# Kernel tuning notes

Measured on AMD Instinct MI355X. Metric: run time of the kernel, lower is better.

## Reference

```python
import jax, jax.numpy as jnp
import numpy as np

SCALE = 56  # output spatial resolution, HW = 3136
K = 3       # n_neighbors for top-k softmin scoring


def avg_pool3(x):
    # F.avg_pool2d(x, 3, 1, 1) with count_include_pad=True -> zero-padded sum / 9
    s = jax.lax.reduce_window(x, 0.0, jax.lax.add, (1, 1, 3, 3), (1, 1, 1, 1),
                              ((0, 0), (0, 0), (1, 1), (1, 1)))
    return s / 9.0


def resize_to(x, hw):
    # F.interpolate(mode='bilinear', align_corners=False) == jax.image half-pixel bilinear
    B, C, _, _ = x.shape
    return jax.image.resize(x, (B, C, hw, hw), method='bilinear')


def add_coords(x):
    # CoordConv AddCoords: append normalized x/y coordinate channels in [-1, 1]
    B, C, H, W = x.shape
    xx = jnp.broadcast_to(jnp.linspace(-1.0, 1.0, W, dtype=x.dtype)[None, :], (H, W))
    yy = jnp.broadcast_to(jnp.linspace(-1.0, 1.0, H, dtype=x.dtype)[:, None], (H, W))
    xxb = jnp.broadcast_to(xx[None, None], (B, 1, H, W))
    yyb = jnp.broadcast_to(yy[None, None], (B, 1, H, W))
    return jnp.concatenate([x, xxb, yyb], axis=1)


def setup_inputs() -> dict:
    key = jax.random.key(0)
    k1, k2, k3, k4, k5 = jax.random.split(key, 5)
    p1 = jax.random.normal(k1, (8, 256, 56, 56), dtype=jnp.float32)
    p2 = jax.random.normal(k2, (8, 512, 28, 28), dtype=jnp.float32)
    p3 = jax.random.normal(k3, (8, 1024, 14, 14), dtype=jnp.float32)
    W = jax.random.normal(k4, (1792, 1794), dtype=jnp.float32) * 0.02  # 1x1 CoordConv weight
    b = jnp.zeros((1792,), dtype=jnp.float32)
    C = jax.random.normal(k5, (1792, 3136), dtype=jnp.float32) * 0.05  # centroid bank
    return {"p1": p1, "p2": p2, "p3": p3, "W": W, "b": b, "C": C}


def reference(p1, p2, p3, W, b, C):
    # Descriptor: smooth each pyramid level, upsample to 56x56, concat -> (B,1792,56,56)
    o1 = avg_pool3(p1)
    o2 = resize_to(avg_pool3(p2), SCALE)
    o3 = resize_to(avg_pool3(p3), SCALE)
    sample = jnp.concatenate([o1, o2, o3], axis=1)
    # CoordConv 1x1
    xc = add_coords(sample)  # (B, 1794, 56, 56)
    phi = jnp.einsum('bchw,oc->bohw', xc, W) + b[None, :, None, None]
    B = phi.shape[0]
    phi_p = phi.reshape(B, 1792, SCALE * SCALE).transpose(0, 2, 1)  # (B, HW, C)
    # pairwise squared distances via expansion + matmul: (B, HW, 3136)
    features = jnp.sum(phi_p * phi_p, axis=2, keepdims=True)
    centers = jnp.sum(C * C, axis=0, keepdims=True)
    dist = features + centers - 2.0 * jnp.matmul(phi_p, C)
    dist = jnp.sqrt(jnp.maximum(dist, 0.0))
    # top-K smallest distances (ascending, like torch.topk(largest=False))
    vals = -jax.lax.top_k(-dist, K)[0]  # (B, HW, K)
    w = jax.nn.softmax(-vals, axis=-1)  # softmin
    score = w[..., 0] * vals[..., 0]    # (B, HW)
    score = score.reshape(B, 1, SCALE, SCALE)
    return score
```

## Files before the change

kernel.cpp:

```cpp
#include <hip/hip_runtime.h>
#include <math.h>
#include <stdint.h>

typedef float f32x4 __attribute__((ext_vector_type(4)));
typedef short short8 __attribute__((ext_vector_type(8)));

static constexpr int HWo   = 3136;
static constexpr int NB    = 8;
static constexpr int NP    = 3200;
static constexpr int KDIM  = 1794;
static constexpr int KP1   = 1856;
static constexpr int ODIM  = 1792;
static constexpr int NCENT = 3136;
static constexpr int NHB   = 50;
static constexpr int NHBV  = 49;

__device__ __forceinline__ uint16_t f2bf(float f) {
  union { float f; uint32_t u; } v; v.f = f;
  uint32_t u = v.u;
  return (uint16_t)((u + 0x7FFFu + ((u >> 16) & 1u)) >> 16);
}
__device__ __forceinline__ float bf2f(uint16_t h) {
  union { uint32_t u; float f; } v; v.u = ((uint32_t)h) << 16;
  return v.f;
}

__device__ __forceinline__ void gld16(const uint16_t* __restrict__ g, uint16_t* l) {
  __builtin_amdgcn_global_load_lds(
      (const __attribute__((address_space(1))) uint16_t*)g,
      (__attribute__((address_space(3))) uint16_t*)l,
      16, 0, 0);
}

__device__ __forceinline__ int xcd_swizzle(int bid, int nwg) {
  int q = nwg >> 3, r = nwg & 7;
  int xcd = bid & 7, idx = bid >> 3;
  int base = (xcd < r) ? xcd * (q + 1) : r * (q + 1) + (xcd - r) * q;
  return base + idx;
}

__global__ __launch_bounds__(256) void convW_kernel(const float* __restrict__ W, uint16_t* __restrict__ Wh) {
  int idx = blockIdx.x * 256 + threadIdx.x;
  int o = idx / KP1, k = idx % KP1;
  float v = (k < KDIM) ? W[(size_t)o * KDIM + k] : 0.f;
  Wh[idx] = f2bf(v);
}

__global__ __launch_bounds__(256) void convC_kernel(const float* __restrict__ C, uint16_t* __restrict__ Ct) {
  __shared__ float tile[64][65];
  int bj = blockIdx.x * 64;
  int bo = blockIdx.y * 64;
  int tx = threadIdx.x & 63, ty = threadIdx.x >> 6;
  #pragma unroll
  for (int s = 0; s < 16; ++s) {
    int o = ty + s * 4;
    tile[o][tx] = C[(size_t)(bo + o) * NCENT + bj + tx];
  }
  __syncthreads();
  #pragma unroll
  for (int s = 0; s < 16; ++s) {
    int j = ty + s * 4;
    Ct[(size_t)(bj + j) * ODIM + bo + tx] = f2bf(tile[tx][j]);
  }
}

__global__ __launch_bounds__(256) void rownorm_kernel(const uint16_t* __restrict__ src, float* __restrict__ dst) {
  int t = threadIdx.x, lane = t & 63, wave = t >> 6;
  int row = blockIdx.x * 4 + wave;
  const uint32_t* p = (const uint32_t*)(src + (size_t)row * ODIM);
  float s = 0.f;
  #pragma unroll
  for (int it = 0; it < 14; ++it) {
    uint32_t u = p[it * 64 + lane];
    float a = bf2f((uint16_t)(u & 0xFFFF)), b = bf2f((uint16_t)(u >> 16));
    s += a * a + b * b;
  }
  #pragma unroll
  for (int m = 1; m < 64; m <<= 1) s += __shfl_xor(s, m, 64);
  if (lane == 0) dst[row] = s;
}

__global__ __launch_bounds__(256) void zerof_kernel(float* __restrict__ p, int n) {
  int i = blockIdx.x * 256 + threadIdx.x;
  if (i < n) p[i] = 0.f;
}

static constexpr int P1SZ = 256 * 3136;
static constexpr int P2SZ = 512 * 784;
static constexpr int P3SZ = 1024 * 196;
static constexpr int PTOT = P1SZ + P2SZ + P3SZ;

__device__ __forceinline__ float pool9f(const float* __restrict__ p, int S, int y, int x) {
  float s = 0.f;
  for (int dy = -1; dy <= 1; ++dy) {
    int yy = y + dy; if (yy < 0 || yy >= S) continue;
    for (int dx = -1; dx <= 1; ++dx) {
      int xx = x + dx; if (xx < 0 || xx >= S) continue;
      s += p[yy * S + xx];
    }
  }
  return s * (1.f / 9.f);
}

__global__ __launch_bounds__(256) void pool_kernel(const float* __restrict__ p1, const float* __restrict__ p2,
                                                   const float* __restrict__ p3, float* __restrict__ pooled, int g0) {
  int b = g0 + blockIdx.y;
  float* pb = pooled + (size_t)blockIdx.y * PTOT;
  int idx = blockIdx.x * 256 + threadIdx.x;
  const float* src; int S, loc;
  if (idx < P1SZ)              { src = p1 + (size_t)b * P1SZ; S = 56; loc = idx; }
  else if (idx < P1SZ + P2SZ)  { src = p2 + (size_t)b * P2SZ; S = 28; loc = idx - P1SZ; }
  else                         { src = p3 + (size_t)b * P3SZ; S = 14; loc = idx - P1SZ - P2SZ; }
  int c = loc / (S * S), hw = loc % (S * S);
  pb[idx] = pool9f(src + (size_t)c * S * S, S, hw / S, hw % S);
}

__global__ __launch_bounds__(256) void asmA_kernel(const float* __restrict__ pooled, uint16_t* __restrict__ xcb) {
  __shared__ float tile[64][65];
  int bg = blockIdx.z;
  const float* pb = pooled + (size_t)bg * PTOT;
  uint16_t* xb = xcb + (size_t)bg * NP * KP1;
  int p0 = blockIdx.x * 64;
  int c0 = blockIdx.y * 64;
  int tx = threadIdx.x & 63, ty = threadIdx.x >> 6;
  #pragma unroll
  for (int s = 0; s < 16; ++s) {
    int c = ty + s * 4;
    tile[c][tx] = pb[(size_t)(c0 + c) * HWo + p0 + tx];
  }
  __syncthreads();
  #pragma unroll
  for (int s = 0; s < 16; ++s) {
    int p = ty + s * 4;
    xb[(size_t)(p0 + p) * KP1 + c0 + tx] = f2bf(tile[tx][p]);
  }
}

__global__ __launch_bounds__(256) void asmB_kernel(const float* __restrict__ pooled, uint16_t* __restrict__ xcb) {
  __shared__ float rows[2][128][29];
  int bg = blockIdx.z;
  const float* pb = pooled + (size_t)bg * PTOT;
  uint16_t* xb = xcb + (size_t)bg * NP * KP1;
  int y = blockIdx.x;
  int ct = blockIdx.y;
  bool lvl2 = ct < 4;
  int S = lvl2 ? 28 : 14;
  float scale = lvl2 ? 0.5f : 0.25f;
  float shift = lvl2 ? -0.25f : -0.375f;
  int chbase = lvl2 ? 256 + ct * 128 : 768 + (ct - 4) * 128;
  const float* base = lvl2 ? pb + P1SZ + (size_t)(ct * 128) * 784
                           : pb + P1SZ + P2SZ + (size_t)((ct - 4) * 128) * 196;
  int planesz = S * S;
  float sy = y * scale + shift;
  float fy0 = floorf(sy);
  float fy = sy - fy0;
  int y0 = (int)fy0, y1 = y0 + 1;
  y0 = y0 < 0 ? 0 : y0; y1 = y1 > S - 1 ? S - 1 : y1;
  int t = threadIdx.x;
  int tot = 128 * 2 * S;
  for (int idx = t; idx < tot; idx += 256) {
    int r = idx / S, e = idx - r * S;
    int c = r >> 1, yr = r & 1;
    rows[yr][c][e] = base[(size_t)c * planesz + (yr ? y1 : y0) * S + e];
  }
  __syncthreads();
  int c = t & 127, xs = t >> 7;
  #pragma unroll
  for (int xi = 0; xi < 28; ++xi) {
    int x = xi * 2 + xs;
    float sx = x * scale + shift;
    float fx0 = floorf(sx);
    float fx = sx - fx0;
    int x0 = (int)fx0, x1 = x0 + 1;
    x0 = x0 < 0 ? 0 : x0; x1 = x1 > S - 1 ? S - 1 : x1;
    float v00 = rows[0][c][x0], v01 = rows[0][c][x1];
    float v10 = rows[1][c][x0], v11 = rows[1][c][x1];
    float v = (1.f - fy) * ((1.f - fx) * v00 + fx * v01) + fy * ((1.f - fx) * v10 + fx * v11);
    xb[(size_t)(y * 56 + x) * KP1 + chbase + c] = f2bf(v);
  }
}

__global__ __launch_bounds__(256) void asmC_kernel(uint16_t* __restrict__ xcb) {
  int bg = blockIdx.y;
  uint16_t* xb = xcb + (size_t)bg * NP * KP1;
  int idx = blockIdx.x * 256 + threadIdx.x;
  int i = idx >> 6, ch = 1792 + (idx & 63);
  int x = i % 56, y = i / 56;
  float v = (ch == 1792) ? (-1.f + 2.f * x / 55.f)
          : (ch == 1793) ? (-1.f + 2.f * y / 55.f) : 0.f;
  xb[(size_t)i * KP1 + ch] = f2bf(v);
}

__global__ __launch_bounds__(256) void gemm1_mfma(const uint16_t* __restrict__ Wh, const float* __restrict__ bias,
                                                  const uint16_t* __restrict__ xcb, uint16_t* __restrict__ phi_t,
                                                  float* __restrict__ feat) {
  __shared__ union { uint16_t ab[2][128][64]; uint16_t tr[128][136]; } sm;
  int wid = xcd_swizzle(blockIdx.x, gridDim.x);
  int row0 = (wid % 14) * 128;
  int col0 = (wid / 14) * 128;
  int t = threadIdx.x;
  int lane = t & 63, wave = t >> 6;
  int wm = wave & 1, wn = wave >> 1;
  int l15 = lane & 15, quad = lane >> 4;
  int rr = wave * 8 + (lane >> 3);
  int sg = ((lane & 7) ^ (lane >> 3)) * 8;
  f32x4 acc[4][4] = {};
  for (int k0 = 0; k0 < KP1; k0 += 64) {
    #pragma unroll
    for (int i = 0; i < 4; ++i) {
      gld16(&Wh [(size_t)(row0 + i * 32 + rr) * KP1 + k0 + sg], &sm.ab[0][i * 32 + wave * 8][0]);
      gld16(&xcb[(size_t)(col0 + i * 32 + rr) * KP1 + k0 + sg], &sm.ab[1][i * 32 + wave * 8][0]);
    }
    __syncthreads();
    #pragma unroll
    for (int kk = 0; kk < 2; ++kk) {
      short8 a[4], b[4];
      #pragma unroll
      for (int i = 0; i < 4; ++i) {
        int r = wm * 64 + i * 16 + l15;
        a[i] = *(const short8*)&sm.ab[0][r][((quad + 4 * kk) ^ (r & 7)) * 8];
      }
      #pragma unroll
      for (int j = 0; j < 4; ++j) {
        int r = wn * 64 + j * 16 + l15;
        b[j] = *(const short8*)&sm.ab[1][r][((quad + 4 * kk) ^ (r & 7)) * 8];
      }
      #pragma unroll
      for (int i = 0; i < 4; ++i)
        #pragma unroll
        for (int j = 0; j < 4; ++j)
          acc[i][j] = __builtin_amdgcn_mfma_f32_16x16x32_bf16(a[i], b[j], acc[i][j], 0, 0, 0);
    }
    __syncthreads();
  }
  #pragma unroll
  for (int i = 0; i < 4; ++i) {
    int o4 = wm * 64 + i * 16 + quad * 4;
    float4 bv = *(const float4*)&bias[row0 + o4];
    #pragma unroll
    for (int j = 0; j < 4; ++j) {
      int p = wn * 64 + j * 16 + l15;
      ushort4 u;
      u.x = f2bf(acc[i][j][0] + bv.x);
      u.y = f2bf(acc[i][j][1] + bv.y);
      u.z = f2bf(acc[i][j][2] + bv.z);
      u.w = f2bf(acc[i][j][3] + bv.w);
      *(ushort4*)&sm.tr[p][o4] = u;
    }
  }
  __syncthreads();
  int c = t & 15, prb = t >> 4;
  #pragma unroll
  for (int s = 0; s < 8; ++s) {
    int pr = s * 16 + prb;
    uint4 v = *(const uint4*)&sm.tr[pr][c * 8];
    *(uint4*)&phi_t[(size_t)(col0 + pr) * ODIM + row0 + c * 8] = v;
    const uint16_t* pv = (const uint16_t*)&v;
    float ssq = 0.f;
    #pragma unroll
    for (int e = 0; e < 8; ++e) { float f = bf2f(pv[e]); ssq += f * f; }
    #pragma unroll
    for (int m = 1; m < 16; m <<= 1) ssq += __shfl_xor(ssq, m, 16);
    if (c == 0) atomicAdd(&feat[col0 + pr], ssq);
  }
}

__device__ __forceinline__ void ins3(float v, float& a, float& b, float& c) {
  if (v < c) {
    if (v < b) { c = b; if (v < a) { b = a; a = v; } else { b = v; } }
    else { c = v; }
  }
}

__global__ __launch_bounds__(256) void gemm2_mfma(const uint16_t* __restrict__ phi_t, const uint16_t* __restrict__ Ct,
                                                  const float* __restrict__ cent, float* __restrict__ partial) {
  __shared__ uint16_t As[128][64];
  __shared__ uint16_t Bs[128][64];
  int wid = xcd_swizzle(blockIdx.x, gridDim.x);
  int col0 = (wid % 25) * 128;
  int row0 = (wid / 25) * 128;
  int t = threadIdx.x;
  int lane = t & 63, wave = t >> 6;
  int wc = wave & 1;
  int wp = wave >> 1;
  int l15 = lane & 15, quad = lane >> 4;
  int rr = wave * 8 + (lane >> 3);
  int sg = ((lane & 7) ^ (lane >> 3)) * 8;
  f32x4 acc[4][4] = {};
  for (int k0 = 0; k0 < ODIM; k0 += 64) {
    #pragma unroll
    for (int i = 0; i < 4; ++i) {
      gld16(&phi_t[(size_t)(row0 + i * 32 + rr) * ODIM + k0 + sg], &As[i * 32 + wave * 8][0]);
      gld16(&Ct   [(size_t)(col0 + i * 32 + rr) * ODIM + k0 + sg], &Bs[i * 32 + wave * 8][0]);
    }
    __syncthreads();
    #pragma unroll
    for (int kk = 0; kk < 2; ++kk) {
      short8 ac[4], bp[4];
      #pragma unroll
      for (int i = 0; i < 4; ++i) {
        int r = wc * 64 + i * 16 + l15;
        ac[i] = *(const short8*)&Bs[r][((quad + 4 * kk) ^ (r & 7)) * 8];
      }
      #pragma unroll
      for (int j = 0; j < 4; ++j) {
        int r = wp * 64 + j * 16 + l15;
        bp[j] = *(const short8*)&As[r][((quad + 4 * kk) ^ (r & 7)) * 8];
      }
      #pragma unroll
      for (int i = 0; i < 4; ++i)
        #pragma unroll
        for (int j = 0; j < 4; ++j)
          acc[i][j] = __builtin_amdgcn_mfma_f32_16x16x32_bf16(ac[i], bp[j], acc[i][j], 0, 0, 0);
    }
    __syncthreads();
  }
  if (col0 + wc * 64 < NCENT) {
    float4 cv[4];
    #pragma unroll
    for (int i = 0; i < 4; ++i)
      cv[i] = *(const float4*)&cent[col0 + wc * 64 + i * 16 + quad * 4];
    int hb = (col0 >> 6) + wc;
    #pragma unroll
    for (int j = 0; j < 4; ++j) {
      float t0 = 3.4e38f, t1 = 3.4e38f, t2 = 3.4e38f;
      #pragma unroll
      for (int i = 0; i < 4; ++i) {
        float c4[4] = {cv[i].x, cv[i].y, cv[i].z, cv[i].w};
        #pragma unroll
        for (int r = 0; r < 4; ++r)
          ins3(c4[r] - 2.f * acc[i][j][r], t0, t1, t2);
      }
      #pragma unroll
      for (int m = 16; m < 64; m <<= 1) {
        float u0 = __shfl_xor(t0, m, 64);
        float u1 = __shfl_xor(t1, m, 64);
        float u2 = __shfl_xor(t2, m, 64);
        ins3(u0, t0, t1, t2); ins3(u1, t0, t1, t2); ins3(u2, t0, t1, t2);
      }
      if (quad == 0) {
        int pix = row0 + wp * 64 + j * 16 + l15;
        float* pp = &partial[((size_t)pix * NHB + hb) * 3];
        pp[0] = t0; pp[1] = t1; pp[2] = t2;
      }
    }
  }
}

__global__ __launch_bounds__(256) void score_kernel(const float* __restrict__ partial, const float* __restrict__ feat,
                                                    float* __restrict__ out, int g0) {
  int t = threadIdx.x, lane = t & 63, wave = t >> 6;
  int gi = blockIdx.x * 4 + wave;
  int bg = gi / HWo, row = gi - bg * HWo;
  int grow = bg * NP + row;
  float t0 = 3.4e38f, t1 = 3.4e38f, t2 = 3.4e38f;
  if (lane < NHBV) {
    const float* pp = &partial[((size_t)grow * NHB + lane) * 3];
    ins3(pp[0], t0, t1, t2); ins3(pp[1], t0, t1, t2); ins3(pp[2], t0, t1, t2);
  }
  #pragma unroll
  for (int m = 1; m < 64; m <<= 1) {
    float u0 = __shfl_xor(t0, m, 64);
    float u1 = __shfl_xor(t1, m, 64);
    float u2 = __shfl_xor(t2, m, 64);
    ins3(u0, t0, t1, t2); ins3(u1, t0, t1, t2); ins3(u2, t0, t1, t2);
  }
  if (lane == 0) {
    float ft = feat[grow];
    float v0 = sqrtf(fmaxf(ft + t0, 0.f));
    float v1 = sqrtf(fmaxf(ft + t1, 0.f));
    float v2 = sqrtf(fmaxf(ft + t2, 0.f));
    float w0 = 1.f / (1.f + expf(v0 - v1) + expf(v0 - v2));
    out[(size_t)(g0 + bg) * HWo + row] = v0 * w0;
  }
}

extern "C" void kernel_launch(void* const* d_in, const int* in_sizes, int n_in,
                              void* d_out, int out_size, void* d_ws, size_t ws_size,
                              hipStream_t stream) {
  const float* p1   = (const float*)d_in[0];
  const float* p2   = (const float*)d_in[1];
  const float* p3   = (const float*)d_in[2];
  const float* Wm   = (const float*)d_in[3];
  const float* bias = (const float*)d_in[4];
  const float* Cm   = (const float*)d_in[5];
  float* out = (float*)d_out;

  const size_t szWh   = (size_t)ODIM * KP1 * 2;
  const size_t szCt   = (size_t)NP * ODIM * 2;
  const size_t szCent = (size_t)NP * 4;
  const size_t szXcb  = (size_t)NP * KP1 * 2;
  const size_t szPhi  = (size_t)NP * ODIM * 2;
  const size_t szPart = (size_t)NP * NHB * 3 * 4;
  const size_t szFeat = (size_t)NP * 4;
  const size_t fixedSz = szWh + szCt + szCent;
  const size_t perSz   = szXcb + szPhi + szPart + szFeat;
  int GB = 8;
  while (GB > 1 && fixedSz + perSz * (size_t)GB > ws_size) GB >>= 1;

  char* ws = (char*)d_ws;
  size_t off = 0;
  uint16_t* Wh     = (uint16_t*)(ws + off); off += szWh;
  uint16_t* Ct     = (uint16_t*)(ws + off); off += szCt;
  float*    cent   = (float*)(ws + off);    off += szCent;
  uint16_t* xcb    = (uint16_t*)(ws + off); off += szXcb * GB;
  uint16_t* phi_t  = (uint16_t*)(ws + off);
  float*    pooled = (float*)(ws + off);    off += szPhi * GB;
  float*    partial= (float*)(ws + off);    off += szPart * GB;
  float*    feat   = (float*)(ws + off);    off += szFeat * GB;

  convW_kernel<<<(ODIM * KP1) / 256, 256, 0, stream>>>(Wm, Wh);
  convC_kernel<<<dim3(NCENT / 64, ODIM / 64), 256, 0, stream>>>(Cm, Ct);
  rownorm_kernel<<<784, 256, 0, stream>>>(Ct, cent);

  for (int g0 = 0; g0 < NB; g0 += GB) {
    pool_kernel<<<dim3(PTOT / 256, GB), 256, 0, stream>>>(p1, p2, p3, pooled, g0);
    asmA_kernel<<<dim3(HWo / 64, 4, GB), 256, 0, stream>>>(pooled, xcb);
    asmB_kernel<<<dim3(56, 12, GB), 256, 0, stream>>>(pooled, xcb);
    asmC_kernel<<<dim3((HWo * 64) / 256, GB), 256, 0, stream>>>(xcb);
    zerof_kernel<<<(NP * GB) / 256, 256, 0, stream>>>(feat, NP * GB);
    gemm1_mfma<<<GB * 25 * 14, 256, 0, stream>>>(Wh, bias, xcb, phi_t, feat);
    gemm2_mfma<<<GB * 25 * 25, 256, 0, stream>>>(phi_t, Ct, cent, partial);
    score_kernel<<<GB * HWo / 4, 256, 0, stream>>>(partial, feat, out, g0);
  }
}
```

Baseline: 993.4 us.

## Rewrite distance GEMM as 256x256 double-buffered 8-wave pipelined MFMA kernel

```diff
diff --git a/kernel.cpp b/kernel.cpp
--- a/kernel.cpp
+++ b/kernel.cpp
@@ -12,6 +12,7 @@
 static constexpr int KP1   = 1856;
 static constexpr int ODIM  = 1792;
 static constexpr int NCENT = 3136;
+static constexpr int NPC   = 3328;
 static constexpr int NHB   = 50;
 static constexpr int NHBV  = 49;
 
@@ -272,76 +273,139 @@
   }
 }
 
-__global__ __launch_bounds__(256) void gemm2_mfma(const uint16_t* __restrict__ phi_t, const uint16_t* __restrict__ Ct,
-                                                  const float* __restrict__ cent, float* __restrict__ partial) {
-  __shared__ uint16_t As[128][64];
-  __shared__ uint16_t Bs[128][64];
+#define STGA(buf, hh, kofs) { \
+  gld16(gA[hh][0] + (kofs), &lds[buf][0][(hh) * 128 + wave * 8][0]); \
+  gld16(gA[hh][1] + (kofs), &lds[buf][0][(hh) * 128 + 64 + wave * 8][0]); }
+#define STGB(buf, hh, kofs) { \
+  gld16(gB[hh][0] + (kofs), &lds[buf][1][(hh) * 128 + wave * 8][0]); \
+  gld16(gB[hh][1] + (kofs), &lds[buf][1][(hh) * 128 + 64 + wave * 8][0]); }
+#define LDA(buf, fi, kk) (*(const short8*)&lds[buf][0][((fi) >> 2) * 128 + wm * 64 + ((fi) & 3) * 16 + l15][(((quad) + 4 * (kk)) ^ (l15 & 7)) * 8])
+#define LDB(buf, fj, kk) (*(const short8*)&lds[buf][1][((fj) >> 1) * 128 + ((fj) & 1) * 64 + wn * 16 + l15][(((quad) + 4 * (kk)) ^ (l15 & 7)) * 8])
+
+__global__ __launch_bounds__(512) void gemm2_mfma(const uint16_t* __restrict__ phi_t, const uint16_t* __restrict__ Ct,
+                                                  const float* __restrict__ cent, float* __restrict__ partial,
+                                                  int GBNP) {
+  __shared__ uint16_t lds[2][2][256][64];
   int wid = xcd_swizzle(blockIdx.x, gridDim.x);
-  int col0 = (wid % 25) * 128;
-  int row0 = (wid / 25) * 128;
-  int t = threadIdx.x;
-  int lane = t & 63, wave = t >> 6;
-  int wc = wave & 1;
-  int wp = wave >> 1;
+  int cb = wid % 13, pb = wid / 13;
+  int col0 = cb * 256;
+  int row0 = pb * 256;
+  int t = threadIdx.x, lane = t & 63, wave = t >> 6;
+  int wm = wave & 1, wn = wave >> 1;
   int l15 = lane & 15, quad = lane >> 4;
-  int rr = wave * 8 + (lane >> 3);
-  int sg = ((lane & 7) ^ (lane >> 3)) * 8;
-  f32x4 acc[4][4] = {};
-  for (int k0 = 0; k0 < ODIM; k0 += 64) {
-    #pragma unroll
-    for (int i = 0; i < 4; ++i) {
-      gld16(&phi_t[(size_t)(row0 + i * 32 + rr) * ODIM + k0 + sg], &As[i * 32 + wave * 8][0]);
-      gld16(&Ct   [(size_t)(col0 + i * 32 + rr) * ODIM + k0 + sg], &Bs[i * 32 + wave * 8][0]);
-    }
-    __syncthreads();
-    #pragma unroll
-    for (int kk = 0; kk < 2; ++kk) {
-      short8 ac[4], bp[4];
-      #pragma unroll
-      for (int i = 0; i < 4; ++i) {
-        int r = wc * 64 + i * 16 + l15;
-        ac[i] = *(const short8*)&Bs[r][((quad + 4 * kk) ^ (r & 7)) * 8];
-      }
-      #pragma unroll
-      for (int j = 0; j < 4; ++j) {
-        int r = wp * 64 + j * 16 + l15;
-        bp[j] = *(const short8*)&As[r][((quad + 4 * kk) ^ (r & 7)) * 8];
-      }
-      #pragma unroll
-      for (int i = 0; i < 4; ++i)
-        #pragma unroll
-        for (int j = 0; j < 4; ++j)
-          acc[i][j] = __builtin_amdgcn_mfma_f32_16x16x32_bf16(ac[i], bp[j], acc[i][j], 0, 0, 0);
-    }
-    __syncthreads();
-  }
-  if (col0 + wc * 64 < NCENT) {
-    float4 cv[4];
-    #pragma unroll
-    for (int i = 0; i < 4; ++i)
-      cv[i] = *(const float4*)&cent[col0 + wc * 64 + i * 16 + quad * 4];
-    int hb = (col0 >> 6) + wc;
-    #pragma unroll
-    for (int j = 0; j < 4; ++j) {
-      float t0 = 3.4e38f, t1 = 3.4e38f, t2 = 3.4e38f;
-      #pragma unroll
-      for (int i = 0; i < 4; ++i) {
-        float c4[4] = {cv[i].x, cv[i].y, cv[i].z, cv[i].w};
-        #pragma unroll
-        for (int r = 0; r < 4; ++r)
-          ins3(c4[r] - 2.f * acc[i][j][r], t0, t1, t2);
-      }
-      #pragma unroll
-      for (int m = 16; m < 64; m <<= 1) {
-        float u0 = __shfl_xor(t0, m, 64);
-        float u1 = __shfl_xor(t1, m, 64);
-        float u2 = __shfl_xor(t2, m, 64);
-        ins3(u0, t0, t1, t2); ins3(u1, t0, t1, t2); ins3(u2, t0, t1, t2);
-      }
-      if (quad == 0) {
-        int pix = row0 + wp * 64 + j * 16 + l15;
-        float* pp = &partial[((size_t)pix * NHB + hb) * 3];
-        pp[0] = t0; pp[1] = t1; pp[2] = t2;
+  int srow = lane >> 3;
+  int sg = ((lane & 7) ^ srow) * 8;
+  const uint16_t* gA[2][2];
+  const uint16_t* gB[2][2];
+  #pragma unroll
+  for (int hh = 0; hh < 2; ++hh)
+    #pragma unroll
+    for (int i = 0; i < 2; ++i) {
+      int ra = col0 + hh * 128 + i * 64 + wave * 8 + srow;
+      int rb = row0 + hh * 128 + i * 64 + wave * 8 + srow;
+      rb = rb < GBNP ? rb : GBNP - 1;
+      gA[hh][i] = Ct    + (size_t)ra * ODIM + sg;
+      gB[hh][i] = phi_t + (size_t)rb * ODIM + sg;
+    }
+  f32x4 acc[8][4] = {};
+  STGA(0, 0, 0) STGB(0, 0, 0) STGB(0, 1, 0) STGA(0, 1, 0)
+  STGA(1, 0, 64) STGB(1, 0, 64) STGB(1, 1, 64)
+  asm volatile("s_waitcnt vmcnt(6)" ::: "memory");
+  __builtin_amdgcn_s_barrier();
+  for (int kt = 0; kt < 28; ++kt) {
+    int cur = kt & 1, nxt = cur ^ 1;
+    int k1 = (kt + 1) * 64, k2 = (kt + 2) * 64;
+    short8 a0[4][2], a1[4][2], b0[2][2], b1[2][2];
+    #pragma unroll
+    for (int fi = 0; fi < 4; ++fi) { a0[fi][0] = LDA(cur, fi, 0); a0[fi][1] = LDA(cur, fi, 1); }
+    #pragma unroll
+    for (int fj = 0; fj < 2; ++fj) { b0[fj][0] = LDB(cur, fj, 0); b0[fj][1] = LDB(cur, fj, 1); }
+    if (kt + 1 < 28) STGA(nxt, 1, k1)
+    __builtin_amdgcn_s_barrier();
+    __builtin_amdgcn_s_setprio(1);
+    #pragma unroll
+    for (int fi = 0; fi < 4; ++fi)
+      #pragma unroll
+      for (int fj = 0; fj < 2; ++fj)
+        #pragma unroll
+        for (int kk = 0; kk < 2; ++kk)
+          acc[fi][fj] = __builtin_amdgcn_mfma_f32_16x16x32_bf16(a0[fi][kk], b0[fj][kk], acc[fi][fj], 0, 0, 0);
+    __builtin_amdgcn_s_setprio(0);
+    __builtin_amdgcn_s_barrier();
+    #pragma unroll
+    for (int fj = 0; fj < 2; ++fj) { b1[fj][0] = LDB(cur, fj + 2, 0); b1[fj][1] = LDB(cur, fj + 2, 1); }
+    if (kt + 2 < 28) STGA(cur, 0, k2)
+    __builtin_amdgcn_s_barrier();
+    __builtin_amdgcn_s_setprio(1);
+    #pragma unroll
+    for (int fi = 0; fi < 4; ++fi)
+      #pragma unroll
+      for (int fj = 0; fj < 2; ++fj)
+        #pragma unroll
+        for (int kk = 0; kk < 2; ++kk)
+          acc[fi][fj + 2] = __builtin_amdgcn_mfma_f32_16x16x32_bf16(a0[fi][kk], b1[fj][kk], acc[fi][fj + 2], 0, 0, 0);
+    __builtin_amdgcn_s_setprio(0);
+    __builtin_amdgcn_s_barrier();
+    #pragma unroll
+    for (int fi = 0; fi < 4; ++fi) { a1[fi][0] = LDA(cur, fi + 4, 0); a1[fi][1] = LDA(cur, fi + 4, 1); }
+    if (kt + 2 < 28) STGB(cur, 0, k2)
+    __builtin_amdgcn_s_barrier();
+    __builtin_amdgcn_s_setprio(1);
+    #pragma unroll
+    for (int fi = 0; fi < 4; ++fi)
+      #pragma unroll
+      for (int fj = 0; fj < 2; ++fj)
+        #pragma unroll
+        for (int kk = 0; kk < 2; ++kk)
+          acc[fi + 4][fj + 2] = __builtin_amdgcn_mfma_f32_16x16x32_bf16(a1[fi][kk], b1[fj][kk], acc[fi + 4][fj + 2], 0, 0, 0);
+    __builtin_amdgcn_s_setprio(0);
+    __builtin_amdgcn_s_barrier();
+    if (kt + 2 < 28) STGB(cur, 1, k2)
+    __builtin_amdgcn_s_barrier();
+    __builtin_amdgcn_s_setprio(1);
+    #pragma unroll
+    for (int fi = 0; fi < 4; ++fi)
+      #pragma unroll
+      for (int fj = 0; fj < 2; ++fj)
+        #pragma unroll
+        for (int kk = 0; kk < 2; ++kk)
+          acc[fi + 4][fj] = __builtin_amdgcn_mfma_f32_16x16x32_bf16(a1[fi][kk], b0[fj][kk], acc[fi + 4][fj], 0, 0, 0);
+    __builtin_amdgcn_s_setprio(0);
+    if (kt + 2 < 28)      asm volatile("s_waitcnt vmcnt(6)" ::: "memory");
+    else if (kt + 1 < 28) asm volatile("s_waitcnt vmcnt(0)" ::: "memory");
+    __builtin_amdgcn_s_barrier();
+  }
+  #pragma unroll
+  for (int fihi = 0; fihi < 2; ++fihi) {
+    int cbase = col0 + fihi * 128 + wm * 64;
+    if (cbase < NCENT) {
+      int hb = cbase >> 6;
+      float4 cv[4];
+      #pragma unroll
+      for (int f = 0; f < 4; ++f)
+        cv[f] = *(const float4*)&cent[cbase + f * 16 + quad * 4];
+      #pragma unroll
+      for (int fj = 0; fj < 4; ++fj) {
+        float t0 = 3.4e38f, t1 = 3.4e38f, t2 = 3.4e38f;
+        #pragma unroll
+        for (int f = 0; f < 4; ++f) {
+          float c4[4] = {cv[f].x, cv[f].y, cv[f].z, cv[f].w};
+          #pragma unroll
+          for (int r = 0; r < 4; ++r)
+            ins3(c4[r] - 2.f * acc[fihi * 4 + f][fj][r], t0, t1, t2);
+        }
+        #pragma unroll
+        for (int m = 16; m < 64; m <<= 1) {
+          float u0 = __shfl_xor(t0, m, 64);
+          float u1 = __shfl_xor(t1, m, 64);
+          float u2 = __shfl_xor(t2, m, 64);
+          ins3(u0, t0, t1, t2); ins3(u1, t0, t1, t2); ins3(u2, t0, t1, t2);
+        }
+        int pix = row0 + (fj >> 1) * 128 + (fj & 1) * 64 + wn * 16 + l15;
+        if (quad == 0 && pix < GBNP) {
+          float* pp = &partial[((size_t)pix * NHB + hb) * 3];
+          pp[0] = t0; pp[1] = t1; pp[2] = t2;
+        }
       }
     }
   }
@@ -387,8 +451,8 @@
   float* out = (float*)d_out;
 
   const size_t szWh   = (size_t)ODIM * KP1 * 2;
-  const size_t szCt   = (size_t)NP * ODIM * 2;
-  const size_t szCent = (size_t)NP * 4;
+  const size_t szCt   = (size_t)NPC * ODIM * 2;
+  const size_t szCent = (size_t)NPC * 4;
   const size_t szXcb  = (size_t)NP * KP1 * 2;
   const size_t szPhi  = (size_t)NP * ODIM * 2;
   const size_t szPart = (size_t)NP * NHB * 3 * 4;
@@ -411,16 +475,19 @@
 
   convW_kernel<<<(ODIM * KP1) / 256, 256, 0, stream>>>(Wm, Wh);
   convC_kernel<<<dim3(NCENT / 64, ODIM / 64), 256, 0, stream>>>(Cm, Ct);
-  rownorm_kernel<<<784, 256, 0, stream>>>(Ct, cent);
+  zerof_kernel<<<672, 256, 0, stream>>>((float*)(Ct + (size_t)NCENT * ODIM), 172032);
+  rownorm_kernel<<<NPC / 4, 256, 0, stream>>>(Ct, cent);
 
   for (int g0 = 0; g0 < NB; g0 += GB) {
+    int GBNP = GB * NP;
+    int npb = (GBNP + 255) / 256;
     pool_kernel<<<dim3(PTOT / 256, GB), 256, 0, stream>>>(p1, p2, p3, pooled, g0);
     asmA_kernel<<<dim3(HWo / 64, 4, GB), 256, 0, stream>>>(pooled, xcb);
     asmB_kernel<<<dim3(56, 12, GB), 256, 0, stream>>>(pooled, xcb);
     asmC_kernel<<<dim3((HWo * 64) / 256, GB), 256, 0, stream>>>(xcb);
     zerof_kernel<<<(NP * GB) / 256, 256, 0, stream>>>(feat, NP * GB);
     gemm1_mfma<<<GB * 25 * 14, 256, 0, stream>>>(Wh, bias, xcb, phi_t, feat);
-    gemm2_mfma<<<GB * 25 * 25, 256, 0, stream>>>(phi_t, Ct, cent, partial);
+    gemm2_mfma<<<13 * npb, 512, 0, stream>>>(phi_t, Ct, cent, partial, GBNP);
     score_kernel<<<GB * HWo / 4, 256, 0, stream>>>(partial, feat, out, g0);
   }
 }
```

Measured after the change: 1.048 ms. 5.5% more time.
